# Performance work log

Hardware: AMD Instinct MI355X
Metric: run time of the kernel (lower is better)

Reference implementation:

```python
import jax, jax.numpy as jnp
import numpy as np

B = 131072      # batch
IN = 1024       # input_dim
H = 384         # hidden[0]
L = 128         # latent_dim = hidden[1]
K = 32          # slots_k
R = 2           # top_r
TAU = 0.7


def setup_inputs() -> dict:
    key = jax.random.key(0)
    ks = jax.random.split(key, 8)
    s = 0.02
    f32 = jnp.float32
    return {
        "x":  jax.random.normal(ks[0], (B, IN), f32),
        "w1": jax.random.normal(ks[1], (IN, H), f32) * s,
        "b1": jnp.zeros((H,), f32),
        "w2": jax.random.normal(ks[2], (H, L), f32) * s,
        "b2": jnp.zeros((L,), f32),
        "mk": jax.random.normal(ks[3], (K, L), f32) * s,  # memory_keys
        "mv": jax.random.normal(ks[4], (K, L), f32) * s,  # memory_values
        "w3": jax.random.normal(ks[5], (2 * L, H), f32) * s,
        "b3": jnp.zeros((H,), f32),
        "w4": jax.random.normal(ks[6], (H, 1), f32) * s,
        "b4": jnp.zeros((1,), f32),
    }


def reference(x, w1, b1, w2, b2, mk, mv, w3, b3, w4, b4):
    # block_a: Linear -> GELU -> (Dropout=id in eval) -> Linear -> GELU
    z = jax.nn.gelu(x @ w1 + b1, approximate=False)
    z = jax.nn.gelu(z @ w2 + b2, approximate=False)          # [B, L]

    # top-r slot attention over memory bank
    logits = (z @ mk.T) / TAU                                 # [B, K]
    _, idx = jax.lax.top_k(logits, R)                         # [B, R]
    keep = jax.nn.one_hot(idx, K, dtype=logits.dtype).sum(-2) > 0  # [B, K] bool
    masked = jnp.where(keep, logits, -jnp.inf)
    attn = jax.nn.softmax(masked, axis=-1)                    # [B, K]
    mem = attn @ mv                                           # [B, L]

    fused = jnp.concatenate([z, mem], axis=-1)                # [B, 2L]

    # default head: Linear -> GELU -> Linear(.,1)
    h = jax.nn.gelu(fused @ w3 + b3, approximate=False)
    logit = (h @ w4 + b4)[..., 0]                             # [B]
    return jax.nn.sigmoid(logit)
```

## Files before the change

kernel.cpp:

```cpp
#include <hip/hip_runtime.h>

#define BATCH   131072
#define INDIM   1024
#define BM      64
#define BDIM    256
#define NBLK    (BATCH / BM)

#define WT_OFF   0
#define XT0_OFF  49152
#define XT1_OFF  57344
#define Z1_OFF   0
#define W2T_OFF  50176
#define FZ_OFF   0
#define LG_OFF   33792
#define W3T_OFF  33792
#define RP_OFF   0
#define CB_OFF   66560
#define B1S_OFF  (CB_OFF)
#define B2S_OFF  (CB_OFF + 1536)
#define B3S_OFF  (CB_OFF + 2048)
#define W4S_OFF  (CB_OFF + 3584)
#define MKS_OFF  (CB_OFF + 5120)
#define SMEM_BYTES (CB_OFF + 13824)

typedef unsigned short u16;
typedef u16    u16x8  __attribute__((ext_vector_type(8)));
typedef __bf16 bf16x8 __attribute__((ext_vector_type(8)));
typedef float  f32x4  __attribute__((ext_vector_type(4)));

__device__ __forceinline__ u16 f2bf(float f) {
  unsigned u = __float_as_uint(f);
  u += 0x7FFFu + ((u >> 16) & 1u);
  return (u16)(u >> 16);
}

__device__ __forceinline__ float gelu_exact(float v) {
  return 0.5f * v * (1.0f + erff(v * 0.70710678118654752440f));
}

__device__ __forceinline__ f32x4 mfma16(u16x8 a, u16x8 b, f32x4 c) {
  return __builtin_amdgcn_mfma_f32_16x16x32_bf16(
      __builtin_bit_cast(bf16x8, a), __builtin_bit_cast(bf16x8, b), c, 0, 0, 0);
}

__device__ __forceinline__ u16x8 cvt8(float4 a, float4 b) {
  bf16x8 r;
  r[0]=(__bf16)a.x; r[1]=(__bf16)a.y; r[2]=(__bf16)a.z; r[3]=(__bf16)a.w;
  r[4]=(__bf16)b.x; r[5]=(__bf16)b.y; r[6]=(__bf16)b.z; r[7]=(__bf16)b.w;
  return __builtin_bit_cast(u16x8, r);
}

typedef __attribute__((address_space(3))) unsigned int       lds_u32;
typedef __attribute__((address_space(1))) const unsigned int glb_u32;
__device__ __forceinline__ void gload16(const void* g, void* l) {
  __builtin_amdgcn_global_load_lds((glb_u32*)g, (lds_u32*)l, 16, 0, 0);
}

#define BARRIER_VMN(N) do { \
  asm volatile("s_waitcnt vmcnt(" #N ") lgkmcnt(0)" ::: "memory"); \
  __builtin_amdgcn_s_barrier(); \
  __builtin_amdgcn_sched_barrier(0); } while (0)
#define WAIT_VM0 do { \
  asm volatile("s_waitcnt vmcnt(0)" ::: "memory"); \
  __builtin_amdgcn_sched_barrier(0); } while (0)
#define WAIT_LGKM0 asm volatile("s_waitcnt lgkmcnt(0)" ::: "memory")
#define FENCE_SCHED __builtin_amdgcn_sched_barrier(0)

__global__ void prep_kernel(const float* __restrict__ w1, const float* __restrict__ w2,
                            const float* __restrict__ w3, u16* __restrict__ w1s,
                            u16* __restrict__ w2s, u16* __restrict__ w3s) {
  int i = blockIdx.x * 256 + threadIdx.x;
  if (i < 393216) {
    int kt = i / 24576, p = i % 24576;
    int r = p >> 6, q = p & 63, cp = q >> 3, o = q & 7;
    int k = kt * 64 + ((cp ^ (r & 7)) << 3) + o;
    w1s[i] = f2bf(w1[k * 384 + r]);
  } else if (i < 442368) {
    int j = i - 393216;
    int kt = j / 8192, p = j % 8192;
    int r = p >> 6, q = p & 63, cp = q >> 3, o = q & 7;
    int k = kt * 64 + ((cp ^ (r & 7)) << 3) + o;
    w2s[j] = f2bf(w2[k * 128 + r]);
  } else if (i < 540672) {
    int j = i - 442368;
    int kt = j / 12288, p = j % 12288;
    int r = p >> 5, q = p & 31, cp = q >> 3, o = q & 7;
    int k = kt * 32 + ((cp ^ ((r >> 1) & 3)) << 3) + o;
    w3s[j] = f2bf(w3[k * 384 + r]);
  }
}

__global__ __launch_bounds__(BDIM, 2) void fused_kernel(
    const float* __restrict__ x,  const u16* __restrict__ w1s,
    const float* __restrict__ b1, const u16* __restrict__ w2s,
    const float* __restrict__ b2, const float* __restrict__ mkw,
    const float* __restrict__ mvw, const u16* __restrict__ w3s,
    const float* __restrict__ b3, const float* __restrict__ w4,
    const float* __restrict__ b4, float* __restrict__ out) {
  extern __shared__ char smem[];
  u16*   wt  = (u16*)(smem + WT_OFF);
  u16*   z1  = (u16*)(smem + Z1_OFF);
  u16*   w2t = (u16*)(smem + W2T_OFF);
  u16*   fz  = (u16*)(smem + FZ_OFF);
  float* lgs = (float*)(smem + LG_OFF);
  u16*   w3t = (u16*)(smem + W3T_OFF);
  float* b1s = (float*)(smem + B1S_OFF);
  float* b2s = (float*)(smem + B2S_OFF);
  float* b3s = (float*)(smem + B3S_OFF);
  float* w4s = (float*)(smem + W4S_OFF);
  u16*   mks = (u16*)(smem + MKS_OFF);
  float* rowpart = (float*)(smem + RP_OFF);

  const int tid  = threadIdx.x;
  const int lane = tid & 63;
  const int wid  = tid >> 6;
  const int l15  = lane & 15;
  const int g    = lane >> 4;
  const int aswz = l15 & 7;
  const int bsw2 = (l15 >> 1) & 3;
  const int row0 = blockIdx.x * BM;

  const int sr = tid >> 2;
  const int sj = tid & 3;
  const int csw = (2 * sj) ^ (sr & 7);

  u16* wdst = wt + wid * 6144;
  {
    const u16* ws = w1s + wid * 6144 + lane * 8;
    #pragma unroll
    for (int i = 0; i < 12; ++i) gload16(ws + i * 512, wdst + i * 512);
  }
  FENCE_SCHED;
  const float* xq = x + (long)(row0 + sr) * INDIM + sj * 16;
  float4 xr0 = *(const float4*)xq,       xr1 = *(const float4*)(xq + 4),
         xr2 = *(const float4*)(xq + 8), xr3 = *(const float4*)(xq + 12);

  for (int i = tid; i < 384; i += BDIM) b1s[i] = b1[i];
  for (int i = tid; i < 128; i += BDIM) b2s[i] = b2[i];
  for (int i = tid; i < 384; i += BDIM) b3s[i] = b3[i];
  for (int i = tid; i < 384; i += BDIM) w4s[i] = w4[i];
  {
    int r = tid >> 3, cc = (tid & 7) * 16;
    const float4* p = (const float4*)(mkw + r * 128 + cc);
    float4 a = p[0], b = p[1], c = p[2], d = p[3];
    *(u16x8*)(mks + r * 136 + cc)     = cvt8(a, b);
    *(u16x8*)(mks + r * 136 + cc + 8) = cvt8(c, d);
  }
  {
    u16* xn = (u16*)(smem + XT0_OFF);
    u16x8 lo = cvt8(xr0, xr1), hi = cvt8(xr2, xr3);
    *(u16x8*)(xn + sr * 64 + csw * 8)       = lo;
    *(u16x8*)(xn + sr * 64 + (csw ^ 1) * 8) = hi;
  }
  {
    const float* p = xq + 64;
    xr0 = *(const float4*)p;       xr1 = *(const float4*)(p + 4);
    xr2 = *(const float4*)(p + 8); xr3 = *(const float4*)(p + 12);
  }
  BARRIER_VMN(4);

  f32x4 acc[4][6];
  #pragma unroll
  for (int m = 0; m < 4; ++m)
    #pragma unroll
    for (int n = 0; n < 6; ++n) acc[m][n] = (f32x4){0.f, 0.f, 0.f, 0.f};

  for (int kt = 0; kt < 16; ++kt) {
    const u16* xb = (u16*)(smem + ((kt & 1) ? XT1_OFF : XT0_OFF));
    u16x8 af[2][4], bfr[2][6];
    #pragma unroll
    for (int ks = 0; ks < 2; ++ks) {
      const int kc = ((g + 4 * ks) ^ aswz) * 8;
      #pragma unroll
      for (int m = 0; m < 4; ++m)
        af[ks][m] = *(const u16x8*)(xb + (m * 16 + l15) * 64 + kc);
      #pragma unroll
      for (int n = 0; n < 6; ++n)
        bfr[ks][n] = *(const u16x8*)(wt + (wid * 96 + n * 16 + l15) * 64 + kc);
    }
    WAIT_LGKM0;
    if (kt < 15) {
      const u16* ws = w1s + (kt + 1) * 24576 + wid * 6144 + lane * 8;
      #pragma unroll
      for (int i = 0; i < 12; ++i) gload16(ws + i * 512, wdst + i * 512);
      FENCE_SCHED;
      u16* xn = (u16*)(smem + ((kt & 1) ? XT0_OFF : XT1_OFF));
      u16x8 lo = cvt8(xr0, xr1), hi = cvt8(xr2, xr3);
      *(u16x8*)(xn + sr * 64 + csw * 8)       = lo;
      *(u16x8*)(xn + sr * 64 + (csw ^ 1) * 8) = hi;
      if (kt < 14) {
        const float* p = xq + (kt + 2) * 64;
        xr0 = *(const float4*)p;       xr1 = *(const float4*)(p + 4);
        xr2 = *(const float4*)(p + 8); xr3 = *(const float4*)(p + 12);
      }
    }
    __builtin_amdgcn_s_setprio(1);
    #pragma unroll
    for (int ks = 0; ks < 2; ++ks)
      #pragma unroll
      for (int m = 0; m < 4; ++m)
        #pragma unroll
        for (int n = 0; n < 6; ++n)
          acc[m][n] = mfma16(af[ks][m], bfr[ks][n], acc[m][n]);
    __builtin_amdgcn_s_setprio(0);
    if (kt < 14)       BARRIER_VMN(4);
    else if (kt == 14) BARRIER_VMN(0);
  }
  __syncthreads();

  {
    const u16* s2 = w2s + wid * 2048 + lane * 8;
    u16* d2 = w2t + wid * 2048;
    #pragma unroll
    for (int i = 0; i < 4; ++i) gload16(s2 + i * 512, d2 + i * 512);
  }
  #pragma unroll
  for (int m = 0; m < 4; ++m) {
    #pragma unroll
    for (int n = 0; n < 6; ++n) {
      int col = wid * 96 + n * 16 + l15;
      float bias = b1s[col];
      #pragma unroll
      for (int j = 0; j < 4; ++j)
        z1[(m * 16 + g * 4 + j) * 392 + col] = f2bf(gelu_exact(acc[m][n][j] + bias));
    }
  }
  BARRIER_VMN(0);

  f32x4 acc2[4][2];
  #pragma unroll
  for (int m = 0; m < 4; ++m) { acc2[m][0] = (f32x4){0,0,0,0}; acc2[m][1] = (f32x4){0,0,0,0}; }
  for (int kt = 0; kt < 6; ++kt) {
    u16x8 a2f[2][4], b2f[2][2];
    #pragma unroll
    for (int ks = 0; ks < 2; ++ks) {
      #pragma unroll
      for (int m = 0; m < 4; ++m)
        a2f[ks][m] = *(const u16x8*)(z1 + (m * 16 + l15) * 392 + kt * 64 + ks * 32 + g * 8);
      const int kc = ((g + 4 * ks) ^ aswz) * 8;
      #pragma unroll
      for (int n = 0; n < 2; ++n)
        b2f[ks][n] = *(const u16x8*)(w2t + (wid * 32 + n * 16 + l15) * 64 + kc);
    }
    WAIT_LGKM0;
    if (kt < 5) {
      const u16* s2 = w2s + (kt + 1) * 8192 + wid * 2048 + lane * 8;
      u16* d2 = w2t + wid * 2048;
      #pragma unroll
      for (int i = 0; i < 4; ++i) gload16(s2 + i * 512, d2 + i * 512);
    }
    __builtin_amdgcn_s_setprio(1);
    #pragma unroll
    for (int ks = 0; ks < 2; ++ks)
      #pragma unroll
      for (int m = 0; m < 4; ++m)
        #pragma unroll
        for (int n = 0; n < 2; ++n)
          acc2[m][n] = mfma16(a2f[ks][m], b2f[ks][n], acc2[m][n]);
    __builtin_amdgcn_s_setprio(0);
    if (kt < 5) WAIT_VM0;
  }
  __syncthreads();
  #pragma unroll
  for (int m = 0; m < 4; ++m) {
    #pragma unroll
    for (int n = 0; n < 2; ++n) {
      int col = wid * 32 + n * 16 + l15;
      float bias = b2s[col];
      #pragma unroll
      for (int j = 0; j < 4; ++j)
        fz[(m * 16 + g * 4 + j) * 264 + col] = f2bf(gelu_exact(acc2[m][n][j] + bias));
    }
  }
  __syncthreads();

  {
    f32x4 accl[2] = {(f32x4){0,0,0,0}, (f32x4){0,0,0,0}};
    const int alo = (wid * 16 + l15) * 264 + g * 8;
    const int blo = l15 * 136 + g * 8;
    #pragma unroll
    for (int ks = 0; ks < 4; ++ks) {
      u16x8 a  = *(const u16x8*)(fz + alo + ks * 32);
      u16x8 q0 = *(const u16x8*)(mks + blo + ks * 32);
      u16x8 q1 = *(const u16x8*)(mks + blo + 16 * 136 + ks * 32);
      accl[0] = mfma16(a, q0, accl[0]);
      accl[1] = mfma16(a, q1, accl[1]);
    }
    #pragma unroll
    for (int n = 0; n < 2; ++n)
      #pragma unroll
      for (int j = 0; j < 4; ++j)
        lgs[(wid * 16 + g * 4 + j) * 33 + n * 16 + l15] = accl[n][j] * (1.0f / 0.7f);
  }

  {
    int row = tid >> 2, q = tid & 3;
    const float* lp = lgs + row * 33 + q * 8;
    float m1 = -3.4e38f, m2 = -3.4e38f; int i1 = -1, i2 = -1;
    #pragma unroll
    for (int s = 0; s < 8; ++s) {
      float v = lp[s]; int idx = q * 8 + s;
      if (v > m1) { m2 = m1; i2 = i1; m1 = v; i1 = idx; }
      else if (v > m2) { m2 = v; i2 = idx; }
    }
    #pragma unroll
    for (int d = 1; d <= 2; d <<= 1) {
      float om1 = __shfl_xor(m1, d); int oi1 = __shfl_xor(i1, d);
      float om2 = __shfl_xor(m2, d); int oi2 = __shfl_xor(i2, d);
      bool take = (om1 > m1) || (om1 == m1 && oi1 < i1);
      if (take) {
        float nm2; int ni2;
        if (m1 > om2 || (m1 == om2 && i1 < oi2)) { nm2 = m1; ni2 = i1; }
        else { nm2 = om2; ni2 = oi2; }
        m1 = om1; i1 = oi1; m2 = nm2; i2 = ni2;
      } else {
        if (om1 > m2 || (om1 == m2 && oi1 < i2)) { m2 = om1; i2 = oi1; }
      }
    }
    float a1 = 1.0f / (1.0f + expf(m2 - m1));
    float a2 = 1.0f - a1;
    const float4* v1 = (const float4*)(mvw + i1 * 128 + q * 32);
    const float4* v2 = (const float4*)(mvw + i2 * 128 + q * 32);
    #pragma unroll
    for (int c = 0; c < 4; ++c) {
      float4 pa = v1[c * 2], pb = v1[c * 2 + 1];
      float4 ra = v2[c * 2], rb = v2[c * 2 + 1];
      u16x8 o;
      o[0] = f2bf(a1 * pa.x + a2 * ra.x); o[1] = f2bf(a1 * pa.y + a2 * ra.y);
      o[2] = f2bf(a1 * pa.z + a2 * ra.z); o[3] = f2bf(a1 * pa.w + a2 * ra.w);
      o[4] = f2bf(a1 * pb.x + a2 * rb.x); o[5] = f2bf(a1 * pb.y + a2 * rb.y);
      o[6] = f2bf(a1 * pb.z + a2 * rb.z); o[7] = f2bf(a1 * pb.w + a2 * rb.w);
      *(u16x8*)(fz + row * 264 + 128 + q * 32 + c * 8) = o;
    }
  }
  __syncthreads();

  {
    const u16* s3 = w3s + wid * 3072 + lane * 8;
    u16* d3 = w3t + wid * 3072;
    #pragma unroll
    for (int i = 0; i < 6; ++i) gload16(s3 + i * 512, d3 + i * 512);
  }
  f32x4 acc3[4][6];
  #pragma unroll
  for (int m = 0; m < 4; ++m)
    #pragma unroll
    for (int n = 0; n < 6; ++n) acc3[m][n] = (f32x4){0.f, 0.f, 0.f, 0.f};
  for (int kt = 0; kt < 8; ++kt) {
    WAIT_VM0;
    u16x8 a3f[4], b3f[6];
    #pragma unroll
    for (int m = 0; m < 4; ++m)
      a3f[m] = *(const u16x8*)(fz + (m * 16 + l15) * 264 + kt * 32 + g * 8);
    #pragma unroll
    for (int n = 0; n < 6; ++n)
      b3f[n] = *(const u16x8*)(w3t + (wid * 96 + n * 16 + l15) * 32 + (g ^ bsw2) * 8);
    WAIT_LGKM0;
    if (kt < 7) {
      const u16* s3 = w3s + (kt + 1) * 12288 + wid * 3072 + lane * 8;
      u16* d3 = w3t + wid * 3072;
      #pragma unroll
      for (int i = 0; i < 6; ++i) gload16(s3 + i * 512, d3 + i * 512);
    }
    __builtin_amdgcn_s_setprio(1);
    #pragma unroll
    for (int m = 0; m < 4; ++m)
      #pragma unroll
      for (int n = 0; n < 6; ++n)
        acc3[m][n] = mfma16(a3f[m], b3f[n], acc3[m][n]);
    __builtin_amdgcn_s_setprio(0);
  }
  __syncthreads();

  #pragma unroll
  for (int m = 0; m < 4; ++m) {
    float s0 = 0.f, s1 = 0.f, s2 = 0.f, s3 = 0.f;
    #pragma unroll
    for (int n = 0; n < 6; ++n) {
      int col = wid * 96 + n * 16 + l15;
      float bias = b3s[col], wv = w4s[col];
      s0 += gelu_exact(acc3[m][n][0] + bias) * wv;
      s1 += gelu_exact(acc3[m][n][1] + bias) * wv;
      s2 += gelu_exact(acc3[m][n][2] + bias) * wv;
      s3 += gelu_exact(acc3[m][n][3] + bias) * wv;
    }
    #pragma unroll
    for (int d = 1; d < 16; d <<= 1) {
      s0 += __shfl_xor(s0, d); s1 += __shfl_xor(s1, d);
      s2 += __shfl_xor(s2, d); s3 += __shfl_xor(s3, d);
    }
    if (l15 == 0) {
      int rb = m * 16 + g * 4;
      rowpart[(rb + 0) * 4 + wid] = s0;
      rowpart[(rb + 1) * 4 + wid] = s1;
      rowpart[(rb + 2) * 4 + wid] = s2;
      rowpart[(rb + 3) * 4 + wid] = s3;
    }
  }
  __syncthreads();
  if (tid < BM) {
    float lg = rowpart[tid * 4] + rowpart[tid * 4 + 1] + rowpart[tid * 4 + 2] +
               rowpart[tid * 4 + 3] + b4[0];
    out[row0 + tid] = 1.0f / (1.0f + expf(-lg));
  }
}

extern "C" void kernel_launch(void* const* d_in, const int* in_sizes, int n_in,
                              void* d_out, int out_size, void* d_ws, size_t ws_size,
                              hipStream_t stream) {
  const float* x  = (const float*)d_in[0];
  const float* w1 = (const float*)d_in[1];
  const float* b1 = (const float*)d_in[2];
  const float* w2 = (const float*)d_in[3];
  const float* b2 = (const float*)d_in[4];
  const float* mk = (const float*)d_in[5];
  const float* mv = (const float*)d_in[6];
  const float* w3 = (const float*)d_in[7];
  const float* b3 = (const float*)d_in[8];
  const float* w4 = (const float*)d_in[9];
  const float* b4 = (const float*)d_in[10];

  u16* w1s = (u16*)d_ws;
  u16* w2s = w1s + 393216;
  u16* w3s = w1s + 442368;

  prep_kernel<<<2112, 256, 0, stream>>>(w1, w2, w3, w1s, w2s, w3s);

  (void)hipFuncSetAttribute(reinterpret_cast<const void*>(fused_kernel),
                            hipFuncAttributeMaxDynamicSharedMemorySize, SMEM_BYTES);
  fused_kernel<<<NBLK, BDIM, SMEM_BYTES, stream>>>(x, w1s, b1, w2s, b2, mk, mv, w3s,
                                                   b3, w4, b4, (float*)d_out);
}
```

Before: 283.8 us.

## Halve K-tile to 32 and double-buffer W1 tiles with two-stage prefetch

Stage 1 moves from one K=64 weight buffer to two K=32 weight buffers. W1 loads are issued two tiles ahead, overlapping with the x conversion and the MFMAs, and the loop drops the XOR swizzles in LDS. The W2 and W3 loops use matching K=32 tiles without swizzle, and the first W3 prefetch is issued earlier, during the GELU/attention phase. This trades more iterations and barriers, plus likely LDS bank conflicts from the unswizzled 64-byte rows, for deeper overlap of weight loads.

```diff
diff --git a/kernel.cpp b/kernel.cpp
--- a/kernel.cpp
+++ b/kernel.cpp
@@ -6,16 +6,17 @@
 #define BDIM    256
 #define NBLK    (BATCH / BM)
 
-#define WT_OFF   0
+#define WT0_OFF  0
+#define WT1_OFF  24576
 #define XT0_OFF  49152
-#define XT1_OFF  57344
+#define XT1_OFF  53248
 #define Z1_OFF   0
-#define W2T_OFF  50176
+#define W2T_OFF  57344
 #define FZ_OFF   0
 #define LG_OFF   33792
-#define W3T_OFF  33792
+#define W3T_OFF  42240
 #define RP_OFF   0
-#define CB_OFF   66560
+#define CB_OFF   66816
 #define B1S_OFF  (CB_OFF)
 #define B2S_OFF  (CB_OFF + 1536)
 #define B3S_OFF  (CB_OFF + 2048)
@@ -56,37 +57,29 @@
   __builtin_amdgcn_global_load_lds((glb_u32*)g, (lds_u32*)l, 16, 0, 0);
 }
 
-#define BARRIER_VMN(N) do { \
-  asm volatile("s_waitcnt vmcnt(" #N ") lgkmcnt(0)" ::: "memory"); \
-  __builtin_amdgcn_s_barrier(); \
-  __builtin_amdgcn_sched_barrier(0); } while (0)
 #define WAIT_VM0 do { \
   asm volatile("s_waitcnt vmcnt(0)" ::: "memory"); \
   __builtin_amdgcn_sched_barrier(0); } while (0)
 #define WAIT_LGKM0 asm volatile("s_waitcnt lgkmcnt(0)" ::: "memory")
-#define FENCE_SCHED __builtin_amdgcn_sched_barrier(0)
 
 __global__ void prep_kernel(const float* __restrict__ w1, const float* __restrict__ w2,
                             const float* __restrict__ w3, u16* __restrict__ w1s,
                             u16* __restrict__ w2s, u16* __restrict__ w3s) {
   int i = blockIdx.x * 256 + threadIdx.x;
   if (i < 393216) {
-    int kt = i / 24576, p = i % 24576;
-    int r = p >> 6, q = p & 63, cp = q >> 3, o = q & 7;
-    int k = kt * 64 + ((cp ^ (r & 7)) << 3) + o;
-    w1s[i] = f2bf(w1[k * 384 + r]);
+    int t = i / 12288, p = i % 12288;
+    int r = p >> 5, c = p & 31;
+    w1s[i] = f2bf(w1[(t * 32 + c) * 384 + r]);
   } else if (i < 442368) {
     int j = i - 393216;
-    int kt = j / 8192, p = j % 8192;
-    int r = p >> 6, q = p & 63, cp = q >> 3, o = q & 7;
-    int k = kt * 64 + ((cp ^ (r & 7)) << 3) + o;
-    w2s[j] = f2bf(w2[k * 128 + r]);
+    int t = j / 4096, p = j % 4096;
+    int r = p >> 5, c = p & 31;
+    w2s[j] = f2bf(w2[(t * 32 + c) * 128 + r]);
   } else if (i < 540672) {
     int j = i - 442368;
-    int kt = j / 12288, p = j % 12288;
-    int r = p >> 5, q = p & 31, cp = q >> 3, o = q & 7;
-    int k = kt * 32 + ((cp ^ ((r >> 1) & 3)) << 3) + o;
-    w3s[j] = f2bf(w3[k * 384 + r]);
+    int t = j / 12288, p = j % 12288;
+    int r = p >> 5, c = p & 31;
+    w3s[j] = f2bf(w3[(t * 32 + c) * 384 + r]);
   }
 }
 
@@ -98,7 +91,6 @@
     const float* __restrict__ b3, const float* __restrict__ w4,
     const float* __restrict__ b4, float* __restrict__ out) {
   extern __shared__ char smem[];
-  u16*   wt  = (u16*)(smem + WT_OFF);
   u16*   z1  = (u16*)(smem + Z1_OFF);
   u16*   w2t = (u16*)(smem + W2T_OFF);
   u16*   fz  = (u16*)(smem + FZ_OFF);
@@ -116,24 +108,19 @@
   const int wid  = tid >> 6;
   const int l15  = lane & 15;
   const int g    = lane >> 4;
-  const int aswz = l15 & 7;
-  const int bsw2 = (l15 >> 1) & 3;
   const int row0 = blockIdx.x * BM;
 
   const int sr = tid >> 2;
   const int sj = tid & 3;
-  const int csw = (2 * sj) ^ (sr & 7);
-
-  u16* wdst = wt + wid * 6144;
-  {
-    const u16* ws = w1s + wid * 6144 + lane * 8;
-    #pragma unroll
-    for (int i = 0; i < 12; ++i) gload16(ws + i * 512, wdst + i * 512);
-  }
-  FENCE_SCHED;
-  const float* xq = x + (long)(row0 + sr) * INDIM + sj * 16;
-  float4 xr0 = *(const float4*)xq,       xr1 = *(const float4*)(xq + 4),
-         xr2 = *(const float4*)(xq + 8), xr3 = *(const float4*)(xq + 12);
+
+  {
+    const u16* ws = w1s + wid * 3072 + lane * 8;
+    u16* wd = (u16*)(smem + WT0_OFF) + wid * 3072;
+    #pragma unroll
+    for (int i = 0; i < 6; ++i) gload16(ws + i * 512, wd + i * 512);
+  }
+  const float* xq = x + (long)(row0 + sr) * INDIM + sj * 8;
+  float4 xr0 = *(const float4*)xq, xr1 = *(const float4*)(xq + 4);
 
   for (int i = tid; i < 384; i += BDIM) b1s[i] = b1[i];
   for (int i = tid; i < 128; i += BDIM) b2s[i] = b2[i];
@@ -146,18 +133,17 @@
     *(u16x8*)(mks + r * 136 + cc)     = cvt8(a, b);
     *(u16x8*)(mks + r * 136 + cc + 8) = cvt8(c, d);
   }
-  {
-    u16* xn = (u16*)(smem + XT0_OFF);
-    u16x8 lo = cvt8(xr0, xr1), hi = cvt8(xr2, xr3);
-    *(u16x8*)(xn + sr * 64 + csw * 8)       = lo;
-    *(u16x8*)(xn + sr * 64 + (csw ^ 1) * 8) = hi;
-  }
-  {
-    const float* p = xq + 64;
-    xr0 = *(const float4*)p;       xr1 = *(const float4*)(p + 4);
-    xr2 = *(const float4*)(p + 8); xr3 = *(const float4*)(p + 12);
-  }
-  BARRIER_VMN(4);
+  *(u16x8*)((u16*)(smem + XT0_OFF) + sr * 32 + sj * 8) = cvt8(xr0, xr1);
+  {
+    const u16* ws = w1s + 12288 + wid * 3072 + lane * 8;
+    u16* wd = (u16*)(smem + WT1_OFF) + wid * 3072;
+    #pragma unroll
+    for (int i = 0; i < 6; ++i) gload16(ws + i * 512, wd + i * 512);
+  }
+  { const float* p = xq + 32; xr0 = *(const float4*)p; xr1 = *(const float4*)(p + 4); }
+  asm volatile("s_waitcnt vmcnt(8) lgkmcnt(0)" ::: "memory");
+  __builtin_amdgcn_s_barrier();
+  __builtin_amdgcn_sched_barrier(0);
 
   f32x4 acc[4][6];
   #pragma unroll
@@ -165,54 +151,85 @@
     #pragma unroll
     for (int n = 0; n < 6; ++n) acc[m][n] = (f32x4){0.f, 0.f, 0.f, 0.f};
 
-  for (int kt = 0; kt < 16; ++kt) {
+  for (int kt = 0; kt < 30; ++kt) {
     const u16* xb = (u16*)(smem + ((kt & 1) ? XT1_OFF : XT0_OFF));
-    u16x8 af[2][4], bfr[2][6];
-    #pragma unroll
-    for (int ks = 0; ks < 2; ++ks) {
-      const int kc = ((g + 4 * ks) ^ aswz) * 8;
-      #pragma unroll
-      for (int m = 0; m < 4; ++m)
-        af[ks][m] = *(const u16x8*)(xb + (m * 16 + l15) * 64 + kc);
-      #pragma unroll
-      for (int n = 0; n < 6; ++n)
-        bfr[ks][n] = *(const u16x8*)(wt + (wid * 96 + n * 16 + l15) * 64 + kc);
-    }
+    const u16* wb = (u16*)(smem + ((kt & 1) ? WT1_OFF : WT0_OFF));
+    u16x8 af[4], bfr[6];
+    #pragma unroll
+    for (int m = 0; m < 4; ++m) af[m] = *(const u16x8*)(xb + (m * 16 + l15) * 32 + g * 8);
+    #pragma unroll
+    for (int n = 0; n < 6; ++n)
+      bfr[n] = *(const u16x8*)(wb + (wid * 96 + n * 16 + l15) * 32 + g * 8);
     WAIT_LGKM0;
-    if (kt < 15) {
-      const u16* ws = w1s + (kt + 1) * 24576 + wid * 6144 + lane * 8;
-      #pragma unroll
-      for (int i = 0; i < 12; ++i) gload16(ws + i * 512, wdst + i * 512);
-      FENCE_SCHED;
+    {
+      const u16* ws = w1s + (kt + 2) * 12288 + wid * 3072 + lane * 8;
+      u16* wd = (u16*)(smem + ((kt & 1) ? WT1_OFF : WT0_OFF)) + wid * 3072;
+      #pragma unroll
+      for (int i = 0; i < 6; ++i) gload16(ws + i * 512, wd + i * 512);
+    }
+    __builtin_amdgcn_s_setprio(1);
+    #pragma unroll
+    for (int m = 0; m < 4; ++m)
+      #pragma unroll
+      for (int n = 0; n < 6; ++n) acc[m][n] = mfma16(af[m], bfr[n], acc[m][n]);
+    __builtin_amdgcn_s_setprio(0);
+    {
       u16* xn = (u16*)(smem + ((kt & 1) ? XT0_OFF : XT1_OFF));
-      u16x8 lo = cvt8(xr0, xr1), hi = cvt8(xr2, xr3);
-      *(u16x8*)(xn + sr * 64 + csw * 8)       = lo;
-      *(u16x8*)(xn + sr * 64 + (csw ^ 1) * 8) = hi;
-      if (kt < 14) {
-        const float* p = xq + (kt + 2) * 64;
-        xr0 = *(const float4*)p;       xr1 = *(const float4*)(p + 4);
-        xr2 = *(const float4*)(p + 8); xr3 = *(const float4*)(p + 12);
-      }
-    }
+      *(u16x8*)(xn + sr * 32 + sj * 8) = cvt8(xr0, xr1);
+    }
+    {
+      const float* p = xq + (kt + 2) * 32;
+      xr0 = *(const float4*)p; xr1 = *(const float4*)(p + 4);
+    }
+    asm volatile("s_waitcnt vmcnt(8) lgkmcnt(0)" ::: "memory");
+    __builtin_amdgcn_s_barrier();
+    __builtin_amdgcn_sched_barrier(0);
+  }
+  {
+    const u16* xb = (u16*)(smem + XT0_OFF);
+    const u16* wb = (u16*)(smem + WT0_OFF);
+    u16x8 af[4], bfr[6];
+    #pragma unroll
+    for (int m = 0; m < 4; ++m) af[m] = *(const u16x8*)(xb + (m * 16 + l15) * 32 + g * 8);
+    #pragma unroll
+    for (int n = 0; n < 6; ++n)
+      bfr[n] = *(const u16x8*)(wb + (wid * 96 + n * 16 + l15) * 32 + g * 8);
+    WAIT_LGKM0;
     __builtin_amdgcn_s_setprio(1);
     #pragma unroll
-    for (int ks = 0; ks < 2; ++ks)
-      #pragma unroll
-      for (int m = 0; m < 4; ++m)
-        #pragma unroll
-        for (int n = 0; n < 6; ++n)
-          acc[m][n] = mfma16(af[ks][m], bfr[ks][n], acc[m][n]);
+    for (int m = 0; m < 4; ++m)
+      #pragma unroll
+      for (int n = 0; n < 6; ++n) acc[m][n] = mfma16(af[m], bfr[n], acc[m][n]);
     __builtin_amdgcn_s_setprio(0);
-    if (kt < 14)       BARRIER_VMN(4);
-    else if (kt == 14) BARRIER_VMN(0);
-  }
-  __syncthreads();
-
-  {
-    const u16* s2 = w2s + wid * 2048 + lane * 8;
-    u16* d2 = w2t + wid * 2048;
-    #pragma unroll
-    for (int i = 0; i < 4; ++i) gload16(s2 + i * 512, d2 + i * 512);
+    {
+      u16* xn = (u16*)(smem + XT1_OFF);
+      *(u16x8*)(xn + sr * 32 + sj * 8) = cvt8(xr0, xr1);
+    }
+    asm volatile("s_waitcnt vmcnt(0) lgkmcnt(0)" ::: "memory");
+    __builtin_amdgcn_s_barrier();
+    __builtin_amdgcn_sched_barrier(0);
+  }
+  {
+    const u16* xb = (u16*)(smem + XT1_OFF);
+    const u16* wb = (u16*)(smem + WT1_OFF);
+    u16x8 af[4], bfr[6];
+    #pragma unroll
+    for (int m = 0; m < 4; ++m) af[m] = *(const u16x8*)(xb + (m * 16 + l15) * 32 + g * 8);
+    #pragma unroll
+    for (int n = 0; n < 6; ++n)
+      bfr[n] = *(const u16x8*)(wb + (wid * 96 + n * 16 + l15) * 32 + g * 8);
+    WAIT_LGKM0;
+    #pragma unroll
+    for (int m = 0; m < 4; ++m)
+      #pragma unroll
+      for (int n = 0; n < 6; ++n) acc[m][n] = mfma16(af[m], bfr[n], acc[m][n]);
+  }
+  __syncthreads();
+
+  {
+    const u16* s2 = w2s + wid * 1024 + lane * 8;
+    gload16(s2, w2t + wid * 1024);
+    gload16(s2 + 512, w2t + wid * 1024 + 512);
   }
   #pragma unroll
   for (int m = 0; m < 4; ++m) {
@@ -225,42 +242,41 @@
         z1[(m * 16 + g * 4 + j) * 392 + col] = f2bf(gelu_exact(acc[m][n][j] + bias));
     }
   }
-  BARRIER_VMN(0);
+  __syncthreads();
 
   f32x4 acc2[4][2];
   #pragma unroll
   for (int m = 0; m < 4; ++m) { acc2[m][0] = (f32x4){0,0,0,0}; acc2[m][1] = (f32x4){0,0,0,0}; }
-  for (int kt = 0; kt < 6; ++kt) {
-    u16x8 a2f[2][4], b2f[2][2];
-    #pragma unroll
-    for (int ks = 0; ks < 2; ++ks) {
-      #pragma unroll
-      for (int m = 0; m < 4; ++m)
-        a2f[ks][m] = *(const u16x8*)(z1 + (m * 16 + l15) * 392 + kt * 64 + ks * 32 + g * 8);
-      const int kc = ((g + 4 * ks) ^ aswz) * 8;
-      #pragma unroll
-      for (int n = 0; n < 2; ++n)
-        b2f[ks][n] = *(const u16x8*)(w2t + (wid * 32 + n * 16 + l15) * 64 + kc);
-    }
+  for (int kt = 0; kt < 12; ++kt) {
+    WAIT_VM0;
+    u16x8 a2f[4], b2f[2];
+    #pragma unroll
+    for (int m = 0; m < 4; ++m)
+      a2f[m] = *(const u16x8*)(z1 + (m * 16 + l15) * 392 + kt * 32 + g * 8);
+    #pragma unroll
+    for (int n = 0; n < 2; ++n)
+      b2f[n] = *(const u16x8*)(w2t + (wid * 32 + n * 16 + l15) * 32 + g * 8);
     WAIT_LGKM0;
-    if (kt < 5) {
-      const u16* s2 = w2s + (kt + 1) * 8192 + wid * 2048 + lane * 8;
-      u16* d2 = w2t + wid * 2048;
-      #pragma unroll
-      for (int i = 0; i < 4; ++i) gload16(s2 + i * 512, d2 + i * 512);
+    if (kt < 11) {
+      const u16* s2 = w2s + (kt + 1) * 4096 + wid * 1024 + lane * 8;
+      gload16(s2, w2t + wid * 1024);
+      gload16(s2 + 512, w2t + wid * 1024 + 512);
     }
     __builtin_amdgcn_s_setprio(1);
     #pragma unroll
-    for (int ks = 0; ks < 2; ++ks)
-      #pragma unroll
-      for (int m = 0; m < 4; ++m)
-        #pragma unroll
-        for (int n = 0; n < 2; ++n)
-          acc2[m][n] = mfma16(a2f[ks][m], b2f[ks][n], acc2[m][n]);
+    for (int m = 0; m < 4; ++m)
+      #pragma unroll
+      for (int n = 0; n < 2; ++n) acc2[m][n] = mfma16(a2f[m], b2f[n], acc2[m][n]);
     __builtin_amdgcn_s_setprio(0);
-    if (kt < 5) WAIT_VM0;
-  }
-  __syncthreads();
+  }
+  __syncthreads();
+
+  {
+    const u16* s3 = w3s + wid * 3072 + lane * 8;
+    u16* d3 = w3t + wid * 3072;
+    #pragma unroll
+    for (int i = 0; i < 6; ++i) gload16(s3 + i * 512, d3 + i * 512);
+  }
   #pragma unroll
   for (int m = 0; m < 4; ++m) {
     #pragma unroll
@@ -335,12 +351,6 @@
   }
   __syncthreads();
 
-  {
-    const u16* s3 = w3s + wid * 3072 + lane * 8;
-    u16* d3 = w3t + wid * 3072;
-    #pragma unroll
-    for (int i = 0; i < 6; ++i) gload16(s3 + i * 512, d3 + i * 512);
-  }
   f32x4 acc3[4][6];
   #pragma unroll
   for (int m = 0; m < 4; ++m)
@@ -354,7 +364,7 @@
       a3f[m] = *(const u16x8*)(fz + (m * 16 + l15) * 264 + kt * 32 + g * 8);
     #pragma unroll
     for (int n = 0; n < 6; ++n)
-      b3f[n] = *(const u16x8*)(w3t + (wid * 96 + n * 16 + l15) * 32 + (g ^ bsw2) * 8);
+      b3f[n] = *(const u16x8*)(w3t + (wid * 96 + n * 16 + l15) * 32 + g * 8);
     WAIT_LGKM0;
     if (kt < 7) {
       const u16* s3 = w3s + (kt + 1) * 12288 + wid * 3072 + lane * 8;
@@ -366,8 +376,7 @@
     #pragma unroll
     for (int m = 0; m < 4; ++m)
       #pragma unroll
-      for (int n = 0; n < 6; ++n)
-        acc3[m][n] = mfma16(a3f[m], b3f[n], acc3[m][n]);
+      for (int n = 0; n < 6; ++n) acc3[m][n] = mfma16(a3f[m], b3f[n], acc3[m][n]);
     __builtin_amdgcn_s_setprio(0);
   }
   __syncthreads();
```

After: 319.4 us. 1.13x slower.
